# Kernel tuning notes

Hardware: AMD Instinct MI355X
Metric: run time of the kernel (lower is better)

Reference implementation:

```python
import jax, jax.numpy as jnp
import numpy as np

B, S, D_MODEL, N_HEADS, D_FEAT = 8, 1024, 1024, 16, 64


def setup_inputs() -> dict:
    key = jax.random.key(0)
    ks = jax.random.split(key, 5)
    sin = jax.random.normal(ks[0], (B, S, D_MODEL), dtype=jnp.float32)
    mask = jnp.ones((B, S), dtype=bool)  # only its presence matters in the original
    # Per-head Linear(d_model -> d_feature): weight stored as [H, d_model, d_feature]
    lim = 1.0 / np.sqrt(D_MODEL)
    Wx = jax.random.uniform(ks[1], (N_HEADS, D_MODEL, D_FEAT), dtype=jnp.float32, minval=-lim, maxval=lim)
    bx = jax.random.uniform(ks[2], (N_HEADS, D_FEAT), dtype=jnp.float32, minval=-lim, maxval=lim)
    # Output projection Linear(H*d_feature -> d_model), stored as [in, out]
    lim_p = 1.0 / np.sqrt(N_HEADS * D_FEAT)
    Wp = jax.random.uniform(ks[3], (N_HEADS * D_FEAT, D_MODEL), dtype=jnp.float32, minval=-lim_p, maxval=lim_p)
    bp = jax.random.uniform(ks[4], (D_MODEL,), dtype=jnp.float32, minval=-lim_p, maxval=lim_p)
    return {"sin": sin, "mask": mask, "Wx": Wx, "bx": bx, "Wp": Wp, "bp": bp}


def reference(sin, mask, Wx, bx, Wp, bp):
    # All heads batched: per-head linear projection  [B,H,S,F]
    x = jnp.einsum("bsd,hdf->bhsf", sin, Wx) + bx[None, :, None, :]
    # Cosine-similarity scores: x x^T / (||x|| ||x||^T)  -> [B,H,S,S]
    norm = jnp.sqrt(jnp.sum(x * x, axis=-1, keepdims=True))  # [B,H,S,1]
    scores = jnp.einsum("bhsf,bhtf->bhst", x, x) / (norm * jnp.swapaxes(norm, -2, -1))
    # Original quirk: when mask is not None, entries that are exactly 0.0 get -inf
    scores = jnp.where(scores == 0.0, -jnp.inf, scores)
    p_attn = jax.nn.softmax(scores, axis=-1)
    out = jnp.einsum("bhst,bhtf->bhsf", p_attn, x)
    # Concat heads: [B,S,H*F]
    out = jnp.transpose(out, (0, 2, 1, 3)).reshape(out.shape[0], out.shape[2], -1)
    return out @ Wp + bp
```

## Files before the change

### kernel.cpp

```cpp
#include <hip/hip_runtime.h>
#include <hip/hip_bf16.h>
#include <math.h>

typedef _Float16 f16;
typedef _Float16 half8 __attribute__((ext_vector_type(8)));
typedef float f32x4 __attribute__((ext_vector_type(4)));
typedef float f32x16 __attribute__((ext_vector_type(16)));
typedef unsigned int u32;

#define NB 8
#define NS 1024
#define DM 1024
#define NH 16
#define NF 64

__global__ __launch_bounds__(256) void csin_kernel(const float* __restrict__ in, f16* __restrict__ out) {
  long gid = (long)blockIdx.x * 256 + threadIdx.x;
  const float4* p = (const float4*)(in + gid * 8);
  float4 a = p[0], b = p[1];
  half8 v;
  v[0] = (f16)a.x; v[1] = (f16)a.y; v[2] = (f16)a.z; v[3] = (f16)a.w;
  v[4] = (f16)b.x; v[5] = (f16)b.y; v[6] = (f16)b.z; v[7] = (f16)b.w;
  *(half8*)(out + gid * 8) = v;
}

__global__ __launch_bounds__(256) void cwx_kernel(const float* __restrict__ Wx, f16* __restrict__ W2T) {
  __shared__ float T[64][65];
  int h = blockIdx.x >> 4, d0 = (blockIdx.x & 15) * 64;
  int tid = threadIdx.x;
  const float* src = Wx + ((size_t)h * 1024 + d0) * 64;
  int row = tid >> 2, cg = (tid & 3) * 16;
#pragma unroll
  for (int k = 0; k < 4; ++k) {
    float4 v = *(const float4*)(src + (size_t)row * 64 + cg + k * 4);
    T[row][cg + k * 4 + 0] = v.x;
    T[row][cg + k * 4 + 1] = v.y;
    T[row][cg + k * 4 + 2] = v.z;
    T[row][cg + k * 4 + 3] = v.w;
  }
  __syncthreads();
  int f = tid >> 2, dg = (tid & 3) * 16;
  f16 o[16];
#pragma unroll
  for (int j = 0; j < 16; ++j) o[j] = (f16)T[dg + j][f];
  *(half8*)(W2T + (size_t)(h * 64 + f) * DM + d0 + dg) = *(half8*)&o[0];
  *(half8*)(W2T + (size_t)(h * 64 + f) * DM + d0 + dg + 8) = *(half8*)&o[8];
}

__global__ __launch_bounds__(256) void cwp_kernel(const float* __restrict__ Wp, f16* __restrict__ WpT) {
  __shared__ float T[64][65];
  int n0 = (blockIdx.x >> 4) * 64, d0 = (blockIdx.x & 15) * 64;
  int tid = threadIdx.x;
  int row = tid >> 2, cg = (tid & 3) * 16;
#pragma unroll
  for (int k = 0; k < 4; ++k) {
    float4 v = *(const float4*)(Wp + (size_t)(d0 + row) * DM + n0 + cg + k * 4);
    T[row][cg + k * 4 + 0] = v.x;
    T[row][cg + k * 4 + 1] = v.y;
    T[row][cg + k * 4 + 2] = v.z;
    T[row][cg + k * 4 + 3] = v.w;
  }
  __syncthreads();
  int f = tid >> 2, dg = (tid & 3) * 16;
  f16 o[16];
#pragma unroll
  for (int j = 0; j < 16; ++j) o[j] = (f16)T[dg + j][f];
  *(half8*)(WpT + (size_t)(n0 + f) * DM + d0 + dg) = *(half8*)&o[0];
  *(half8*)(WpT + (size_t)(n0 + f) * DM + d0 + dg + 8) = *(half8*)&o[8];
}

template <int MODE>
__global__ __launch_bounds__(256) void gemm_kernel(const f16* __restrict__ A, const f16* __restrict__ Bt,
                                                   const float* __restrict__ bias, void* __restrict__ Cv) {
  __shared__ f16 As[128][64];
  __shared__ f16 Bs[128][64];
  int tid = threadIdx.x;
  int l = tid & 63, wv = tid >> 6;
  int wm = wv >> 1, wn = wv & 1;
  int xcd = blockIdx.x & 7, m = blockIdx.x >> 3;
  int bm = ((m >> 3) << 3) | xcd;
  int bn = m & 7;
  int lr = l & 15, lh = l >> 4;

  f32x4 acc[4][4];
#pragma unroll
  for (int i = 0; i < 4; ++i)
#pragma unroll
    for (int j = 0; j < 4; ++j) acc[i][j] = (f32x4)0.f;

  const f16* gA = A + (size_t)(bm * 128 + wv * 32 + (l >> 3)) * DM + (l & 7) * 8;
  const f16* gB = Bt + (size_t)(bn * 128 + wv * 32 + (l >> 3)) * DM + (l & 7) * 8;
  f16* ldsA = &As[wv * 32][0];
  f16* ldsB = &Bs[wv * 32][0];

  for (int k0 = 0; k0 < DM; k0 += 64) {
    __syncthreads();
#pragma unroll
    for (int c = 0; c < 4; ++c) {
      __builtin_amdgcn_global_load_lds(
          (const __attribute__((address_space(1))) void*)(gA + k0 + (size_t)c * 8 * DM),
          (__attribute__((address_space(3))) void*)(ldsA + c * 512), 16, 0, 0);
      __builtin_amdgcn_global_load_lds(
          (const __attribute__((address_space(1))) void*)(gB + k0 + (size_t)c * 8 * DM),
          (__attribute__((address_space(3))) void*)(ldsB + c * 512), 16, 0, 0);
    }
    __syncthreads();
#pragma unroll
    for (int ks = 0; ks < 2; ++ks) {
      half8 af[4], bf[4];
#pragma unroll
      for (int mi = 0; mi < 4; ++mi) af[mi] = *(const half8*)&As[wm * 64 + mi * 16 + lr][ks * 32 + lh * 8];
#pragma unroll
      for (int ni = 0; ni < 4; ++ni) bf[ni] = *(const half8*)&Bs[wn * 64 + ni * 16 + lr][ks * 32 + lh * 8];
#pragma unroll
      for (int mi = 0; mi < 4; ++mi)
#pragma unroll
        for (int ni = 0; ni < 4; ++ni)
          acc[mi][ni] = __builtin_amdgcn_mfma_f32_16x16x32_f16(af[mi], bf[ni], acc[mi][ni], 0, 0, 0);
    }
  }

#pragma unroll
  for (int mi = 0; mi < 4; ++mi)
#pragma unroll
    for (int ni = 0; ni < 4; ++ni) {
      int gc = bn * 128 + wn * 64 + ni * 16 + lr;
      float bv = bias[gc];
#pragma unroll
      for (int r = 0; r < 4; ++r) {
        int gr = bm * 128 + wm * 64 + mi * 16 + lh * 4 + r;
        float v = acc[mi][ni][r] + bv;
        if (MODE == 0) {
          f16* x = (f16*)Cv;
          int b = gr >> 10, s = gr & 1023, h = gc >> 6, f = gc & 63;
          x[(size_t)((b * NH + h) * NS + s) * NF + f] = (f16)v;
        } else {
          ((float*)Cv)[(size_t)gr * DM + gc] = v;
        }
      }
    }
}

__global__ __launch_bounds__(256) void transnorm_kernel(f16* __restrict__ x, f16* __restrict__ xT) {
  __shared__ f16 T[64][64];
  __shared__ float sinv[64];
  int bh = blockIdx.x >> 4, s0 = (blockIdx.x & 15) * 64;
  int tid = threadIdx.x;
  f16* xb = x + (size_t)bh * (NS * NF);
  half8 vv[2];
#pragma unroll
  for (int it = 0; it < 2; ++it) {
    int idx = it * 256 + tid;
    int sr = idx >> 3, fcb = idx & 7;
    half8 v = *(const half8*)(xb + (size_t)(s0 + sr) * NF + fcb * 8);
    vv[it] = v;
    *(half8*)&T[sr][((fcb ^ ((sr >> 3) & 7)) * 8)] = v;
    float s = 0.f;
#pragma unroll
    for (int j = 0; j < 8; ++j) {
      float u = (float)v[j];
      s += u * u;
    }
    s += __shfl_xor(s, 1, 64);
    s += __shfl_xor(s, 2, 64);
    s += __shfl_xor(s, 4, 64);
    if ((tid & 7) == 0) sinv[sr] = rsqrtf(s);
  }
  __syncthreads();
#pragma unroll
  for (int it = 0; it < 2; ++it) {
    int idx = it * 256 + tid;
    int fr = idx >> 3, scb = idx & 7;
    half8 v;
#pragma unroll
    for (int j = 0; j < 8; ++j) v[j] = T[scb * 8 + j][(((fr >> 3) ^ scb) * 8) + (fr & 7)];
    *(half8*)(xT + ((size_t)bh * NF + fr) * NS + s0 + scb * 8) = v;
  }
#pragma unroll
  for (int it = 0; it < 2; ++it) {
    int idx = it * 256 + tid;
    int sr = idx >> 3, fcb = idx & 7;
    float inv = sinv[sr];
    half8 v = vv[it], o;
#pragma unroll
    for (int j = 0; j < 8; ++j) o[j] = (f16)((float)v[j] * inv);
    *(half8*)(xb + (size_t)(s0 + sr) * NF + fcb * 8) = o;
  }
}

__global__ __launch_bounds__(256) void attn_kernel(const f16* __restrict__ xn, const f16* __restrict__ xT,
                                                   f16* __restrict__ ao) {
  __shared__ f16 KB[2][2048];
  __shared__ f16 VB[2][2048];

  int tid = threadIdx.x;
  int l = tid & 63, wv = tid >> 6;
  int lq = l & 31, hi = l >> 5;
  int kq = hi * 8;
  int xcd = blockIdx.x & 7, m = blockIdx.x >> 3;
  int bh = ((m >> 2) << 3) | xcd;
  int q0 = (m & 3) * 256;
  const f16* xnb = xn + (size_t)bh * (NS * NF);
  const f16* xTb = xT + (size_t)bh * (NF * NS);

  int krow = wv * 8 + (l >> 3);
  const f16* gK0 = xnb + (size_t)krow * NF + (((l & 7) ^ (krow & 7)) * 8);
  int vrow = wv * 16 + (l >> 2);
  const f16* gV0 = xTb + (size_t)vrow * NS + (((l & 3) ^ (vrow & 3)) * 8);

  int akoff[4], vboff[2][2];
#pragma unroll
  for (int ks = 0; ks < 4; ++ks)
    akoff[ks] = lq * 128 + ((((ks * 2 + hi)) ^ (lq & 7)) << 4);
#pragma unroll
  for (int sub = 0; sub < 2; ++sub)
#pragma unroll
    for (int ni = 0; ni < 2; ++ni) {
      int r = ni * 32 + lq;
      vboff[sub][ni] = r * 64 + (((sub * 2 + hi) ^ (r & 3)) << 4);
    }

  half8 bq[2][4];
#pragma unroll
  for (int qs = 0; qs < 2; ++qs)
#pragma unroll
    for (int ks = 0; ks < 4; ++ks)
      bq[qs][ks] = *(const half8*)(xnb + (size_t)(q0 + wv * 64 + qs * 32 + lq) * NF + ks * 16 + kq);

  f32x16 accO[2][2];
  accO[0][0] = (f32x16)0.f;
  accO[0][1] = (f32x16)0.f;
  accO[1][0] = (f32x16)0.f;
  accO[1][1] = (f32x16)0.f;
  float rs[2] = {0.f, 0.f};

#define STAGE(buf, t0_)                                                                              \
  do {                                                                                               \
    __builtin_amdgcn_global_load_lds(                                                                \
        (const __attribute__((address_space(1))) void*)(gK0 + (size_t)(t0_) * NF),                   \
        (__attribute__((address_space(3))) void*)(&KB[buf][wv * 512]), 16, 0, 0);                    \
    __builtin_amdgcn_global_load_lds(                                                                \
        (const __attribute__((address_space(1))) void*)(gV0 + (t0_)),                                \
        (__attribute__((address_space(3))) void*)(&VB[buf][wv * 512]), 16, 0, 0);                    \
  } while (0)

  const float L2E = 1.4426950408889634f;

  STAGE(0, 0);
  asm volatile("s_waitcnt vmcnt(0)" ::: "memory");
  __syncthreads();

  int cur = 0;
  for (int t = 0; t < 32; ++t) {
    if (t < 31) STAGE(cur ^ 1, (t + 1) * 32);

    const char* kb = (const char*)&KB[cur][0];
    const char* vb = (const char*)&VB[cur][0];
    half8 ak[4];
#pragma unroll
    for (int ks = 0; ks < 4; ++ks) ak[ks] = *(const half8*)(kb + akoff[ks]);
    half8 vbl[2][2];
#pragma unroll
    for (int sub = 0; sub < 2; ++sub)
#pragma unroll
      for (int ni = 0; ni < 2; ++ni) vbl[sub][ni] = *(const half8*)(vb + vboff[sub][ni]);

#pragma unroll
    for (int qs = 0; qs < 2; ++qs) {
      f32x16 sa = (f32x16)0.f;
      __builtin_amdgcn_s_setprio(1);
#pragma unroll
      for (int ks = 0; ks < 4; ++ks)
        sa = __builtin_amdgcn_mfma_f32_32x32x16_f16(ak[ks], bq[qs][ks], sa, 0, 0, 0);
      __builtin_amdgcn_s_setprio(0);

      u32 pk[8];
#pragma unroll
      for (int mm = 0; mm < 8; ++mm) {
        float a = sa[2 * mm], b = sa[2 * mm + 1];
        float ea = (a == 0.f) ? 0.f : exp2f(__builtin_fmaf(a, L2E, -L2E));
        float eb = (b == 0.f) ? 0.f : exp2f(__builtin_fmaf(b, L2E, -L2E));
        rs[qs] += ea + eb;
        auto h = __builtin_amdgcn_cvt_pkrtz(ea, eb);
        pk[mm] = __builtin_bit_cast(u32, h);
      }
      uint4 a0, a1;
#if __has_builtin(__builtin_amdgcn_permlane32_swap)
      {
        auto s02 = __builtin_amdgcn_permlane32_swap((int)pk[0], (int)pk[2], false, false);
        auto s13 = __builtin_amdgcn_permlane32_swap((int)pk[1], (int)pk[3], false, false);
        auto s46 = __builtin_amdgcn_permlane32_swap((int)pk[4], (int)pk[6], false, false);
        auto s57 = __builtin_amdgcn_permlane32_swap((int)pk[5], (int)pk[7], false, false);
        a0.x = (u32)s02[0]; a0.z = (u32)s02[1];
        a0.y = (u32)s13[0]; a0.w = (u32)s13[1];
        a1.x = (u32)s46[0]; a1.z = (u32)s46[1];
        a1.y = (u32)s57[0]; a1.w = (u32)s57[1];
      }
#else
      {
        u32 sw[8];
#pragma unroll
        for (int mm = 0; mm < 8; ++mm) sw[mm] = (u32)__shfl_xor((int)pk[mm], 32, 64);
        bool lo = (hi == 0);
        a0.x = lo ? pk[0] : sw[2];
        a0.y = lo ? pk[1] : sw[3];
        a0.z = lo ? sw[0] : pk[2];
        a0.w = lo ? sw[1] : pk[3];
        a1.x = lo ? pk[4] : sw[6];
        a1.y = lo ? pk[5] : sw[7];
        a1.z = lo ? sw[4] : pk[6];
        a1.w = lo ? sw[5] : pk[7];
      }
#endif
      half8 pa0 = __builtin_bit_cast(half8, a0);
      half8 pa1 = __builtin_bit_cast(half8, a1);
      __builtin_amdgcn_s_setprio(1);
#pragma unroll
      for (int sub = 0; sub < 2; ++sub) {
        half8 pa = sub ? pa1 : pa0;
#pragma unroll
        for (int ni = 0; ni < 2; ++ni)
          accO[qs][ni] = __builtin_amdgcn_mfma_f32_32x32x16_f16(pa, vbl[sub][ni], accO[qs][ni], 0, 0, 0);
      }
      __builtin_amdgcn_s_setprio(0);
    }

    asm volatile("s_waitcnt vmcnt(0)" ::: "memory");
    __syncthreads();
    cur ^= 1;
  }
#undef STAGE

  rs[0] += __shfl_xor(rs[0], 32, 64);
  rs[1] += __shfl_xor(rs[1], 32, 64);

  int b = bh >> 4, h = bh & 15;
#pragma unroll
  for (int qs = 0; qs < 2; ++qs)
#pragma unroll
    for (int r = 0; r < 16; ++r) {
      int qoff = (r & 3) + 8 * (r >> 2) + 4 * hi;
      float rv = __shfl(rs[qs], qoff, 64);
      float rinv = 1.0f / rv;
      int qg = q0 + wv * 64 + qs * 32 + qoff;
#pragma unroll
      for (int ni = 0; ni < 2; ++ni) {
        int f = ni * 32 + lq;
        ao[((size_t)(b * NS + qg)) * DM + h * NF + f] = (f16)(accO[qs][ni][r] * rinv);
      }
    }
}

extern "C" void kernel_launch(void* const* d_in, const int* in_sizes, int n_in,
                              void* d_out, int out_size, void* d_ws, size_t ws_size,
                              hipStream_t stream) {
  const float* sin_in = (const float*)d_in[0];
  const float* Wx = (const float*)d_in[2];
  const float* bx = (const float*)d_in[3];
  const float* Wp = (const float*)d_in[4];
  const float* bp = (const float*)d_in[5];
  float* out = (float*)d_out;

  char* p = (char*)d_ws;
  f16* sinb = (f16*)p;                      p += (size_t)NB * NS * DM * 2;
  f16* x    = (f16*)p;                      p += (size_t)NB * NH * NS * NF * 2;
  f16* xT   = (f16*)p;                      p += (size_t)NB * NH * NF * NS * 2;
  f16* W2T  = (f16*)p;                      p += (size_t)DM * DM * 2;
  f16* WpT  = (f16*)p;                      p += (size_t)DM * DM * 2;
  f16* ao   = sinb;

  csin_kernel<<<4096, 256, 0, stream>>>(sin_in, sinb);
  cwx_kernel<<<256, 256, 0, stream>>>(Wx, W2T);
  cwp_kernel<<<256, 256, 0, stream>>>(Wp, WpT);
  gemm_kernel<0><<<512, 256, 0, stream>>>(sinb, W2T, bx, (void*)x);
  transnorm_kernel<<<2048, 256, 0, stream>>>(x, xT);
  attn_kernel<<<512, 256, 0, stream>>>(x, xT, ao);
  gemm_kernel<1><<<512, 256, 0, stream>>>(ao, WpT, bp, (void*)out);
}
```

Measured before the change: 237.0 us.

## Halve attention query tile per block and double key/value tile per stage

Each attention block now handles 128 queries (32 per wave) instead of 256, so the grid doubles to 1024 blocks. Each pipeline stage now loads 64 keys and values instead of 32, which halves the number of loop iterations and barriers. K and V fragments are read from LDS inside the inner loop rather than preloaded, and launch bounds request 4 blocks per CU. The aim is better occupancy and fewer synchronisations. In exchange, every key/value tile is reloaded by twice as many blocks and LDS use per block doubles.

```diff
diff --git a/kernel.cpp b/kernel.cpp
--- a/kernel.cpp
+++ b/kernel.cpp
@@ -188,60 +188,50 @@
   }
 }
 
-__global__ __launch_bounds__(256) void attn_kernel(const f16* __restrict__ xn, const f16* __restrict__ xT,
-                                                   f16* __restrict__ ao) {
-  __shared__ f16 KB[2][2048];
-  __shared__ f16 VB[2][2048];
+__global__ __launch_bounds__(256, 4) void attn_kernel(const f16* __restrict__ xn, const f16* __restrict__ xT,
+                                                      f16* __restrict__ ao) {
+  __shared__ f16 KB[2][4096];
+  __shared__ f16 VB[2][4096];
 
   int tid = threadIdx.x;
   int l = tid & 63, wv = tid >> 6;
   int lq = l & 31, hi = l >> 5;
   int kq = hi * 8;
   int xcd = blockIdx.x & 7, m = blockIdx.x >> 3;
-  int bh = ((m >> 2) << 3) | xcd;
-  int q0 = (m & 3) * 256;
+  int bh = ((m >> 3) << 3) | xcd;
+  int q0 = (m & 7) * 128;
   const f16* xnb = xn + (size_t)bh * (NS * NF);
   const f16* xTb = xT + (size_t)bh * (NF * NS);
 
-  int krow = wv * 8 + (l >> 3);
-  const f16* gK0 = xnb + (size_t)krow * NF + (((l & 7) ^ (krow & 7)) * 8);
-  int vrow = wv * 16 + (l >> 2);
-  const f16* gV0 = xTb + (size_t)vrow * NS + (((l & 3) ^ (vrow & 3)) * 8);
-
-  int akoff[4], vboff[2][2];
+  int srow = wv * 8 + (l >> 3);
+  int scol = ((l & 7) ^ (l >> 3)) * 8;
+  const f16* gK0 = xnb + (size_t)srow * NF + scol;
+  const f16* gV0 = xTb + (size_t)srow * NS + scol;
+
+  half8 bq[4];
 #pragma unroll
   for (int ks = 0; ks < 4; ++ks)
-    akoff[ks] = lq * 128 + ((((ks * 2 + hi)) ^ (lq & 7)) << 4);
-#pragma unroll
-  for (int sub = 0; sub < 2; ++sub)
-#pragma unroll
-    for (int ni = 0; ni < 2; ++ni) {
-      int r = ni * 32 + lq;
-      vboff[sub][ni] = r * 64 + (((sub * 2 + hi) ^ (r & 3)) << 4);
-    }
-
-  half8 bq[2][4];
-#pragma unroll
-  for (int qs = 0; qs < 2; ++qs)
-#pragma unroll
-    for (int ks = 0; ks < 4; ++ks)
-      bq[qs][ks] = *(const half8*)(xnb + (size_t)(q0 + wv * 64 + qs * 32 + lq) * NF + ks * 16 + kq);
-
-  f32x16 accO[2][2];
-  accO[0][0] = (f32x16)0.f;
-  accO[0][1] = (f32x16)0.f;
-  accO[1][0] = (f32x16)0.f;
-  accO[1][1] = (f32x16)0.f;
-  float rs[2] = {0.f, 0.f};
-
-#define STAGE(buf, t0_)                                                                              \
-  do {                                                                                               \
-    __builtin_amdgcn_global_load_lds(                                                                \
-        (const __attribute__((address_space(1))) void*)(gK0 + (size_t)(t0_) * NF),                   \
-        (__attribute__((address_space(3))) void*)(&KB[buf][wv * 512]), 16, 0, 0);                    \
-    __builtin_amdgcn_global_load_lds(                                                                \
-        (const __attribute__((address_space(1))) void*)(gV0 + (t0_)),                                \
-        (__attribute__((address_space(3))) void*)(&VB[buf][wv * 512]), 16, 0, 0);                    \
+    bq[ks] = *(const half8*)(xnb + (size_t)(q0 + wv * 32 + lq) * NF + ks * 16 + kq);
+
+  f32x16 accO[2];
+  accO[0] = (f32x16)0.f;
+  accO[1] = (f32x16)0.f;
+  float rs = 0.f;
+
+#define STAGE(buf, t0_)                                                                               \
+  do {                                                                                                \
+    __builtin_amdgcn_global_load_lds(                                                                 \
+        (const __attribute__((address_space(1))) void*)(gK0 + (size_t)(t0_) * NF),                    \
+        (__attribute__((address_space(3))) void*)(&KB[buf][wv * 512]), 16, 0, 0);                     \
+    __builtin_amdgcn_global_load_lds(                                                                 \
+        (const __attribute__((address_space(1))) void*)(gK0 + (size_t)(t0_ + 32) * NF),               \
+        (__attribute__((address_space(3))) void*)(&KB[buf][2048 + wv * 512]), 16, 0, 0);              \
+    __builtin_amdgcn_global_load_lds(                                                                 \
+        (const __attribute__((address_space(1))) void*)(gV0 + (t0_)),                                 \
+        (__attribute__((address_space(3))) void*)(&VB[buf][wv * 512]), 16, 0, 0);                     \
+    __builtin_amdgcn_global_load_lds(                                                                 \
+        (const __attribute__((address_space(1))) void*)(gV0 + (size_t)32 * NS + (t0_)),               \
+        (__attribute__((address_space(3))) void*)(&VB[buf][2048 + wv * 512]), 16, 0, 0);              \
   } while (0)
 
   const float L2E = 1.4426950408889634f;
@@ -251,27 +241,24 @@
   __syncthreads();
 
   int cur = 0;
-  for (int t = 0; t < 32; ++t) {
-    if (t < 31) STAGE(cur ^ 1, (t + 1) * 32);
+  for (int t = 0; t < 16; ++t) {
+    if (t < 15) STAGE(cur ^ 1, (t + 1) * 64);
 
     const char* kb = (const char*)&KB[cur][0];
     const char* vb = (const char*)&VB[cur][0];
-    half8 ak[4];
-#pragma unroll
-    for (int ks = 0; ks < 4; ++ks) ak[ks] = *(const half8*)(kb + akoff[ks]);
-    half8 vbl[2][2];
-#pragma unroll
-    for (int sub = 0; sub < 2; ++sub)
-#pragma unroll
-      for (int ni = 0; ni < 2; ++ni) vbl[sub][ni] = *(const half8*)(vb + vboff[sub][ni]);
-
-#pragma unroll
-    for (int qs = 0; qs < 2; ++qs) {
+
+#pragma unroll
+    for (int ti = 0; ti < 2; ++ti) {
+      half8 ak[4];
+#pragma unroll
+      for (int ks = 0; ks < 4; ++ks)
+        ak[ks] = *(const half8*)(kb + (ti * 32 + lq) * 128 + ((((ks * 2 + hi)) ^ (lq & 7)) << 4));
+
       f32x16 sa = (f32x16)0.f;
       __builtin_amdgcn_s_setprio(1);
 #pragma unroll
       for (int ks = 0; ks < 4; ++ks)
-        sa = __builtin_amdgcn_mfma_f32_32x32x16_f16(ak[ks], bq[qs][ks], sa, 0, 0, 0);
+        sa = __builtin_amdgcn_mfma_f32_32x32x16_f16(ak[ks], bq[ks], sa, 0, 0, 0);
       __builtin_amdgcn_s_setprio(0);
 
       u32 pk[8];
@@ -280,7 +267,7 @@
         float a = sa[2 * mm], b = sa[2 * mm + 1];
         float ea = (a == 0.f) ? 0.f : exp2f(__builtin_fmaf(a, L2E, -L2E));
         float eb = (b == 0.f) ? 0.f : exp2f(__builtin_fmaf(b, L2E, -L2E));
-        rs[qs] += ea + eb;
+        rs += ea + eb;
         auto h = __builtin_amdgcn_cvt_pkrtz(ea, eb);
         pk[mm] = __builtin_bit_cast(u32, h);
       }
@@ -319,8 +306,10 @@
       for (int sub = 0; sub < 2; ++sub) {
         half8 pa = sub ? pa1 : pa0;
 #pragma unroll
-        for (int ni = 0; ni < 2; ++ni)
-          accO[qs][ni] = __builtin_amdgcn_mfma_f32_32x32x16_f16(pa, vbl[sub][ni], accO[qs][ni], 0, 0, 0);
+        for (int ni = 0; ni < 2; ++ni) {
+          half8 vbf = *(const half8*)(vb + (ni * 32 + lq) * 128 + (((ti * 4 + sub * 2 + hi) ^ (lq & 7)) << 4));
+          accO[ni] = __builtin_amdgcn_mfma_f32_32x32x16_f16(pa, vbf, accO[ni], 0, 0, 0);
+        }
       }
       __builtin_amdgcn_s_setprio(0);
     }
@@ -331,24 +320,21 @@
   }
 #undef STAGE
 
-  rs[0] += __shfl_xor(rs[0], 32, 64);
-  rs[1] += __shfl_xor(rs[1], 32, 64);
+  rs += __shfl_xor(rs, 32, 64);
 
   int b = bh >> 4, h = bh & 15;
 #pragma unroll
-  for (int qs = 0; qs < 2; ++qs)
-#pragma unroll
-    for (int r = 0; r < 16; ++r) {
-      int qoff = (r & 3) + 8 * (r >> 2) + 4 * hi;
-      float rv = __shfl(rs[qs], qoff, 64);
-      float rinv = 1.0f / rv;
-      int qg = q0 + wv * 64 + qs * 32 + qoff;
-#pragma unroll
-      for (int ni = 0; ni < 2; ++ni) {
-        int f = ni * 32 + lq;
-        ao[((size_t)(b * NS + qg)) * DM + h * NF + f] = (f16)(accO[qs][ni][r] * rinv);
-      }
-    }
+  for (int r = 0; r < 16; ++r) {
+    int qoff = (r & 3) + 8 * (r >> 2) + 4 * hi;
+    float rv = __shfl(rs, qoff, 64);
+    float rinv = 1.0f / rv;
+    int qg = q0 + wv * 32 + qoff;
+#pragma unroll
+    for (int ni = 0; ni < 2; ++ni) {
+      int f = ni * 32 + lq;
+      ao[((size_t)(b * NS + qg)) * DM + h * NF + f] = (f16)(accO[ni][r] * rinv);
+    }
+  }
 }
 
 extern "C" void kernel_launch(void* const* d_in, const int* in_sizes, int n_in,
@@ -374,6 +360,6 @@
   cwp_kernel<<<256, 256, 0, stream>>>(Wp, WpT);
   gemm_kernel<0><<<512, 256, 0, stream>>>(sinb, W2T, bx, (void*)x);
   transnorm_kernel<<<2048, 256, 0, stream>>>(x, xT);
-  attn_kernel<<<512, 256, 0, stream>>>(x, xT, ao);
+  attn_kernel<<<1024, 256, 0, stream>>>(x, xT, ao);
   gemm_kernel<1><<<512, 256, 0, stream>>>(ao, WpT, bp, (void*)out);
 }
```

New measurement: 223.6 us. 1.06x faster.
